# Optimization experiments

Measured on AMD Instinct MI355X. Metric: run time of the kernel, lower is better.

## Reference

```python
import jax, jax.numpy as jnp
import numpy as np

B, CW_DIM, Z_DIM = 512, 4096, 1024
DIM_CODES, BOOK_SIZE, DIM_EMBED = 64, 1024, 64
ENC_H, DEC_H = 512, 2048
SLOPE = 0.2  # LeakyReLU negative slope

def lrelu(v):
    return jnp.where(v > 0, v, SLOPE * v)

def setup_inputs() -> dict:
    key = jax.random.key(0)
    ks = jax.random.split(key, 12)
    s = 0.02
    inp = {
        'x': jax.random.normal(ks[0], (B, CW_DIM), jnp.float32),
        'codebook': jax.random.normal(ks[1], (DIM_CODES, BOOK_SIZE, DIM_EMBED), jnp.float32),
        'enc_w1': jax.random.normal(ks[2], (ENC_H, DIM_EMBED), jnp.float32) * s,
        'enc_b1': jnp.zeros((ENC_H,), jnp.float32),
        'enc_w2': jax.random.normal(ks[3], (2 * Z_DIM, ENC_H), jnp.float32) * s,
        'enc_b2': jnp.zeros((2 * Z_DIM,), jnp.float32),
        'inf1_w': jax.random.normal(ks[4], (Z_DIM // 2, 2 * Z_DIM), jnp.float32) * s,
        'inf1_b': jnp.zeros((Z_DIM // 2,), jnp.float32),
        'inf2_w1': jax.random.normal(ks[5], (2 * Z_DIM, 9 * Z_DIM // 4), jnp.float32) * s,
        'inf2_b1': jnp.zeros((2 * Z_DIM,), jnp.float32),
        'inf2_w2': jax.random.normal(ks[6], (3 * Z_DIM // 2, 2 * Z_DIM), jnp.float32) * s,
        'inf2_b2': jnp.zeros((3 * Z_DIM // 2,), jnp.float32),
        'prior_w1': jax.random.normal(ks[7], (2 * Z_DIM, Z_DIM // 4), jnp.float32) * s,
        'prior_b1': jnp.zeros((2 * Z_DIM,), jnp.float32),
        'prior_w2': jax.random.normal(ks[8], (3 * Z_DIM // 2, 2 * Z_DIM), jnp.float32) * s,
        'prior_b2': jnp.zeros((3 * Z_DIM // 2,), jnp.float32),
        'dec_w1': jax.random.normal(ks[9], (DEC_H, 3 * Z_DIM // 4), jnp.float32) * s,
        'dec_b1': jnp.zeros((DEC_H,), jnp.float32),
        'dec_w2': jax.random.normal(ks[10], (CW_DIM, DEC_H), jnp.float32) * s,
        'dec_b2': jnp.zeros((CW_DIM,), jnp.float32),
    }
    return inp

def reference(x, codebook, enc_w1, enc_b1, enc_w2, enc_b2,
              inf1_w, inf1_b, inf2_w1, inf2_b1, inf2_w2, inf2_b2,
              prior_w1, prior_b1, prior_w2, prior_b2,
              dec_w1, dec_b1, dec_w2, dec_b2):
    b = x.shape[0]
    # ---- encode: view (B, dim_codes, dim_embed), per-code conv + max-pool + Linear
    xe = x.reshape(b, DIM_CODES, DIM_EMBED)                       # (B, C, E)
    feat = lrelu(jnp.einsum('bce,he->bch', xe, enc_w1) + enc_b1)  # (B, C, H)
    h = jnp.max(feat, axis=1) @ enc_w2.T + enc_b2                 # (B, 2z)
    mu, log_var = jnp.split(h @ inf1_w.T + inf1_b, 2, axis=1)     # (B, z/4) each
    z1 = mu                                                        # eval mode: sample == mu
    # ---- decode
    p = lrelu(z1 @ prior_w1.T + prior_b1) @ prior_w2.T + prior_b2
    p_mu, p_logvar = jnp.split(p, 2, axis=1)                       # (B, 3z/4) each
    d = lrelu(jnp.concatenate([z1, h], axis=1) @ inf2_w1.T + inf2_b1) @ inf2_w2.T + inf2_b2
    d_mu, d_log_var = jnp.split(d, 2, axis=1)
    z2 = d_mu + p_mu                                               # eval mode sample
    cw_recon = lrelu(z2 @ dec_w1.T + dec_b1) @ dec_w2.T + dec_b2   # (B, cw_dim)
    # ---- dist: squared distance to (detached) codebook, no explicit repeat
    xr = cw_recon.reshape(b, DIM_CODES, DIM_EMBED)
    book = jax.lax.stop_gradient(codebook)                         # (C, S, E)
    cw_dist = ((xr ** 2).sum(-1)[..., None]
               + (book ** 2).sum(-1)[None]
               - 2.0 * jnp.einsum('bce,cse->bcs', xr, book))       # (B, C, S)
    idx = jnp.argmin(cw_dist, axis=-1).reshape(b * DIM_CODES, 1)   # matches torch (B*C, 1)
    return (cw_recon, cw_dist, idx, mu, log_var, d_mu, d_log_var, p_logvar)
```

## Files before the change

### kernel.cpp

```cpp
#include <hip/hip_runtime.h>
#include <hip/hip_bf16.h>

typedef __hip_bfloat16 bf16;
typedef unsigned short u16;

#define BATCH 512
#define CW_DIM 4096
#define DIM_CODES 64
#define BOOK_SIZE 1024
#define DIM_EMBED 64
#define ENC_H 512

__device__ __forceinline__ float bf2f(u16 u) {
    unsigned int x = ((unsigned int)u) << 16;
    return __uint_as_float(x);
}
__device__ __forceinline__ float loadf(const void* p, size_t i, int bf) {
    if (bf) return bf2f(((const u16*)p)[i]);
    return ((const float*)p)[i];
}
__device__ __forceinline__ float4 load4(const void* p, size_t i, int bf) {
    if (bf) {
        const u16* q = (const u16*)p + i;
        uint2 raw = *reinterpret_cast<const uint2*>(q);
        float4 r;
        r.x = bf2f((u16)(raw.x & 0xFFFF));
        r.y = bf2f((u16)(raw.x >> 16));
        r.z = bf2f((u16)(raw.y & 0xFFFF));
        r.w = bf2f((u16)(raw.y >> 16));
        return r;
    }
    return *reinterpret_cast<const float4*>((const float*)p + i);
}
__device__ __forceinline__ void stored(void* p, size_t i, int bf, double v) {
    if (bf) ((bf16*)p)[i] = __float2bfloat16((float)v);
    else    ((float*)p)[i] = (float)v;
}
__device__ __forceinline__ u16 f2bfu(float v) {
    bf16 b = __float2bfloat16(v);
    return *reinterpret_cast<u16*>(&b);
}

__global__ void detect_kernel(const u16* __restrict__ x, int* __restrict__ flag) {
    __shared__ int hits;
    if (threadIdx.x == 0) hits = 0;
    __syncthreads();
    int h = 0;
    for (int i = threadIdx.x; i < 16384; i += 256) {
        u16 v = x[2 * i];
        if (((v >> 7) & 0xFF) == 0xFF) h++;
    }
    atomicAdd(&hits, h);
    __syncthreads();
    if (threadIdx.x == 0) *flag = (hits == 0) ? 1 : 0;
}

__global__ void booknorm_kernel(const void* __restrict__ book, double* __restrict__ bn,
                                const int* __restrict__ dflag) {
    const int bf = *dflag;
    int r = blockIdx.x * blockDim.x + threadIdx.x;
    if (r >= DIM_CODES * BOOK_SIZE) return;
    double acc = 0.0;
    for (int e = 0; e < DIM_EMBED; e += 4) {
        float4 v = load4(book, (size_t)r * DIM_EMBED + e, bf);
        acc = fma((double)v.x, (double)v.x, acc);
        acc = fma((double)v.y, (double)v.y, acc);
        acc = fma((double)v.z, (double)v.z, acc);
        acc = fma((double)v.w, (double)v.w, acc);
    }
    bn[r] = acc;
}

__global__ __launch_bounds__(256) void enc_kernel(const void* __restrict__ x,
                                                  const void* __restrict__ w1,
                                                  const void* __restrict__ b1,
                                                  float* __restrict__ hmax,
                                                  const int* __restrict__ dflag) {
    const int bf = *dflag;
    __shared__ float xs_t[64][68];
    __shared__ float wsh_t[64][68];
    __shared__ float red[64][17];
    int t = threadIdx.x;
    int h0 = blockIdx.x * 64;
    int b = blockIdx.y;

    int cr = t >> 2;
    int e0 = (t & 3) << 4;
    for (int q = 0; q < 4; q++) {
        int e = e0 + (q << 2);
        float4 xv = load4(x, (size_t)b * CW_DIM + cr * DIM_EMBED + e, bf);
        xs_t[e + 0][cr] = xv.x; xs_t[e + 1][cr] = xv.y;
        xs_t[e + 2][cr] = xv.z; xs_t[e + 3][cr] = xv.w;
        float4 wv = load4(w1, (size_t)(h0 + cr) * DIM_EMBED + e, bf);
        wsh_t[e + 0][cr] = wv.x; wsh_t[e + 1][cr] = wv.y;
        wsh_t[e + 2][cr] = wv.z; wsh_t[e + 3][cr] = wv.w;
    }
    __syncthreads();

    int th = t & 15, tc = t >> 4;
    float acc[4][4] = {};
    for (int e = 0; e < 64; e++) {
        float4 a4 = *(const float4*)&xs_t[e][tc << 2];
        float4 w4 = *(const float4*)&wsh_t[e][th << 2];
        float aa[4] = {a4.x, a4.y, a4.z, a4.w};
        float ww[4] = {w4.x, w4.y, w4.z, w4.w};
#pragma unroll
        for (int i = 0; i < 4; i++)
#pragma unroll
            for (int j = 0; j < 4; j++)
                acc[i][j] = fmaf(aa[i], ww[j], acc[i][j]);
    }
#pragma unroll
    for (int j = 0; j < 4; j++) {
        float bj = loadf(b1, h0 + (th << 2) + j, bf);
        float m = -1e30f;
#pragma unroll
        for (int i = 0; i < 4; i++) {
            float v = acc[i][j] + bj;
            v = v > 0.f ? v : 0.2f * v;
            m = fmaxf(m, v);
        }
        red[(th << 2) + j][tc] = m;
    }
    __syncthreads();
    if (t < 64) {
        float m = red[t][0];
        for (int k = 1; k < 16; k++) m = fmaxf(m, red[t][k]);
        hmax[(size_t)b * ENC_H + h0 + t] = m;
    }
}

struct GDesc {
    const float* A1; const float* A2; const float* Aadd;
    const void* W; const void* bias; float* C;
    int lda1, K1, lda2, Ktot, N, act, nbx, pad;
    size_t s0base; int s0c0, s0c1, s0stride;
    size_t s1base; int s1c0, s1c1, s1stride;
};

__device__ __forceinline__ void gemm_body(const GDesc& g, int bx, int by,
                                          void* __restrict__ out, const int bf) {
    __shared__ float As[2][16][68];
    __shared__ float Ws[2][16][68];
    int t = threadIdx.x;
    int tx = t & 15, ty = t >> 4;
    int n0 = bx * 64, m0 = by * 64;
    int mrow = t >> 2, kq = (t & 3) << 2;
    float acc[4][4] = {};

    float4 av, wv;
    {
        int k = kq;
        if (k < g.K1) {
            av = *reinterpret_cast<const float4*>(g.A1 + (size_t)(m0 + mrow) * g.lda1 + k);
            if (g.Aadd) {
                float4 ad = *reinterpret_cast<const float4*>(g.Aadd + (size_t)(m0 + mrow) * g.lda1 + k);
                av.x += ad.x; av.y += ad.y; av.z += ad.z; av.w += ad.w;
            }
        } else {
            av = *reinterpret_cast<const float4*>(g.A2 + (size_t)(m0 + mrow) * g.lda2 + (k - g.K1));
        }
        wv = load4(g.W, (size_t)(n0 + mrow) * g.Ktot + k, bf);
    }
    As[0][kq + 0][mrow] = av.x; As[0][kq + 1][mrow] = av.y;
    As[0][kq + 2][mrow] = av.z; As[0][kq + 3][mrow] = av.w;
    Ws[0][kq + 0][mrow] = wv.x; Ws[0][kq + 1][mrow] = wv.y;
    Ws[0][kq + 2][mrow] = wv.z; Ws[0][kq + 3][mrow] = wv.w;
    __syncthreads();

    int buf = 0;
#pragma unroll 1
    for (int kt = 0; kt < g.Ktot; kt += 16) {
        int nxt = kt + 16;
        if (nxt < g.Ktot) {
            int k = nxt + kq;
            if (k < g.K1) {
                av = *reinterpret_cast<const float4*>(g.A1 + (size_t)(m0 + mrow) * g.lda1 + k);
                if (g.Aadd) {
                    float4 ad = *reinterpret_cast<const float4*>(g.Aadd + (size_t)(m0 + mrow) * g.lda1 + k);
                    av.x += ad.x; av.y += ad.y; av.z += ad.z; av.w += ad.w;
                }
            } else {
                av = *reinterpret_cast<const float4*>(g.A2 + (size_t)(m0 + mrow) * g.lda2 + (k - g.K1));
            }
            wv = load4(g.W, (size_t)(n0 + mrow) * g.Ktot + k, bf);
        }
#pragma unroll
        for (int kk = 0; kk < 16; kk++) {
            float4 a4 = *(const float4*)&As[buf][kk][ty << 2];
            float4 w4 = *(const float4*)&Ws[buf][kk][tx << 2];
            float a[4] = {a4.x, a4.y, a4.z, a4.w};
            float w[4] = {w4.x, w4.y, w4.z, w4.w};
#pragma unroll
            for (int i = 0; i < 4; i++)
#pragma unroll
                for (int j = 0; j < 4; j++)
                    acc[i][j] = fmaf(a[i], w[j], acc[i][j]);
        }
        if (nxt < g.Ktot) {
            int nb = buf ^ 1;
            As[nb][kq + 0][mrow] = av.x; As[nb][kq + 1][mrow] = av.y;
            As[nb][kq + 2][mrow] = av.z; As[nb][kq + 3][mrow] = av.w;
            Ws[nb][kq + 0][mrow] = wv.x; Ws[nb][kq + 1][mrow] = wv.y;
            Ws[nb][kq + 2][mrow] = wv.z; Ws[nb][kq + 3][mrow] = wv.w;
            __syncthreads();
            buf = nb;
        }
    }

    int nbase = n0 + tx * 4;
    float b0 = loadf(g.bias, nbase + 0, bf), b1v = loadf(g.bias, nbase + 1, bf);
    float b2 = loadf(g.bias, nbase + 2, bf), b3 = loadf(g.bias, nbase + 3, bf);
#pragma unroll
    for (int i = 0; i < 4; i++) {
        int m = m0 + ty * 4 + i;
        float ov[4];
        ov[0] = acc[i][0] + b0; ov[1] = acc[i][1] + b1v;
        ov[2] = acc[i][2] + b2; ov[3] = acc[i][3] + b3;
        if (g.act) {
#pragma unroll
            for (int j = 0; j < 4; j++) ov[j] = ov[j] > 0.f ? ov[j] : 0.2f * ov[j];
        }
        float4 o = {ov[0], ov[1], ov[2], ov[3]};
        *reinterpret_cast<float4*>(g.C + (size_t)m * g.N + nbase) = o;
        if (nbase >= g.s0c0 && nbase < g.s0c1) {
            size_t off = g.s0base + (size_t)m * g.s0stride + (nbase - g.s0c0);
            if (bf) {
                ushort4 h = {f2bfu(ov[0]), f2bfu(ov[1]), f2bfu(ov[2]), f2bfu(ov[3])};
                *reinterpret_cast<ushort4*>((u16*)out + off) = h;
            } else {
                *reinterpret_cast<float4*>((float*)out + off) = o;
            }
        }
        if (nbase >= g.s1c0 && nbase < g.s1c1) {
            size_t off = g.s1base + (size_t)m * g.s1stride + (nbase - g.s1c0);
            if (bf) {
                ushort4 h = {f2bfu(ov[0]), f2bfu(ov[1]), f2bfu(ov[2]), f2bfu(ov[3])};
                *reinterpret_cast<ushort4*>((u16*)out + off) = h;
            } else {
                *reinterpret_cast<float4*>((float*)out + off) = o;
            }
        }
    }
}

__global__ __launch_bounds__(256) void gemm_kernel(GDesc g, void* __restrict__ out,
                                                   const int* __restrict__ dflag) {
    gemm_body(g, blockIdx.x, blockIdx.y, out, *dflag);
}

__global__ __launch_bounds__(256) void gemm2_kernel(GDesc g0, GDesc g1, void* __restrict__ out,
                                                    const int* __restrict__ dflag) {
    const int bf = *dflag;
    bool first = (int)blockIdx.x < g0.nbx;
    GDesc g = first ? g0 : g1;
    int bx = first ? blockIdx.x : blockIdx.x - g0.nbx;
    gemm_body(g, bx, blockIdx.y, out, bf);
}

__global__ __launch_bounds__(256, 4) void dist_kernel(const float* __restrict__ cwr,
                                                      const void* __restrict__ book,
                                                      const double* __restrict__ bn,
                                                      void* __restrict__ out,
                                                      size_t odist, size_t oidx,
                                                      const int* __restrict__ dflag) {
    const int bf = *dflag;
    __shared__ double xs[32][64];
    __shared__ double xn[32];
    __shared__ float bs[2][64][66];
    int t = threadIdx.x;
    int c = blockIdx.x;
    int b0 = blockIdx.y * 32;
    int sl = t & 63, wv = t >> 6;

    for (int i = t; i < 32 * 64; i += 256) {
        int bl = i >> 6, e = i & 63;
        xs[bl][e] = (double)cwr[(size_t)(b0 + bl) * CW_DIM + c * DIM_EMBED + e];
    }
    {
        size_t base = (size_t)c * BOOK_SIZE * DIM_EMBED;
        int i4, srow, e4;
        i4 = t;       srow = i4 >> 4; e4 = (i4 & 15) << 2;
        float4 v0 = load4(book, base + (size_t)srow * DIM_EMBED + e4, bf);
        bs[0][srow][e4 + 0] = v0.x; bs[0][srow][e4 + 1] = v0.y;
        bs[0][srow][e4 + 2] = v0.z; bs[0][srow][e4 + 3] = v0.w;
        i4 = t + 256; srow = i4 >> 4; e4 = (i4 & 15) << 2;
        float4 v1 = load4(book, base + (size_t)srow * DIM_EMBED + e4, bf);
        bs[0][srow][e4 + 0] = v1.x; bs[0][srow][e4 + 1] = v1.y;
        bs[0][srow][e4 + 2] = v1.z; bs[0][srow][e4 + 3] = v1.w;
        i4 = t + 512; srow = i4 >> 4; e4 = (i4 & 15) << 2;
        float4 v2 = load4(book, base + (size_t)srow * DIM_EMBED + e4, bf);
        bs[0][srow][e4 + 0] = v2.x; bs[0][srow][e4 + 1] = v2.y;
        bs[0][srow][e4 + 2] = v2.z; bs[0][srow][e4 + 3] = v2.w;
        i4 = t + 768; srow = i4 >> 4; e4 = (i4 & 15) << 2;
        float4 v3 = load4(book, base + (size_t)srow * DIM_EMBED + e4, bf);
        bs[0][srow][e4 + 0] = v3.x; bs[0][srow][e4 + 1] = v3.y;
        bs[0][srow][e4 + 2] = v3.z; bs[0][srow][e4 + 3] = v3.w;
    }
    __syncthreads();
    if (t < 32) {
        double a = 0.0;
        for (int e = 0; e < 64; e++) a = fma(xs[t][e], xs[t][e], a);
        xn[t] = a;
    }
    __syncthreads();

    double bd[8];
    int bsx[8];
#pragma unroll
    for (int p = 0; p < 8; p++) { bd[p] = 1e300; bsx[p] = 0; }

#pragma unroll 1
    for (int st = 0; st < 16; st++) {
        int s0 = st * 64;
        int cur = st & 1, nb = cur ^ 1;
        double bnv = bn[(size_t)c * BOOK_SIZE + s0 + sl];
        float4 pf0, pf1, pf2, pf3;
        int s0n = s0 + 64;
        if (st < 15) {
            size_t base = ((size_t)c * BOOK_SIZE + s0n) * DIM_EMBED;
            int i4, srow, e4;
            i4 = t;       srow = i4 >> 4; e4 = (i4 & 15) << 2;
            pf0 = load4(book, base + (size_t)srow * DIM_EMBED + e4, bf);
            i4 = t + 256; srow = i4 >> 4; e4 = (i4 & 15) << 2;
            pf1 = load4(book, base + (size_t)srow * DIM_EMBED + e4, bf);
            i4 = t + 512; srow = i4 >> 4; e4 = (i4 & 15) << 2;
            pf2 = load4(book, base + (size_t)srow * DIM_EMBED + e4, bf);
            i4 = t + 768; srow = i4 >> 4; e4 = (i4 & 15) << 2;
            pf3 = load4(book, base + (size_t)srow * DIM_EMBED + e4, bf);
        }
#pragma unroll
        for (int pb = 0; pb < 2; pb++) {
            int blb = wv * 8 + pb * 4;
            double a0 = 0.0, a1 = 0.0, a2 = 0.0, a3 = 0.0;
#pragma unroll 8
            for (int e = 0; e < 64; e += 2) {
                float2 bv = *(const float2*)&bs[cur][sl][e];
                double bv0 = (double)bv.x, bv1 = (double)bv.y;
                double2 x0 = *(const double2*)&xs[blb + 0][e];
                double2 x1 = *(const double2*)&xs[blb + 1][e];
                double2 x2 = *(const double2*)&xs[blb + 2][e];
                double2 x3 = *(const double2*)&xs[blb + 3][e];
                a0 = fma(x0.x, bv0, a0); a0 = fma(x0.y, bv1, a0);
                a1 = fma(x1.x, bv0, a1); a1 = fma(x1.y, bv1, a1);
                a2 = fma(x2.x, bv0, a2); a2 = fma(x2.y, bv1, a2);
                a3 = fma(x3.x, bv0, a3); a3 = fma(x3.y, bv1, a3);
            }
            double dv[4];
            dv[0] = a0; dv[1] = a1; dv[2] = a2; dv[3] = a3;
#pragma unroll
            for (int j = 0; j < 4; j++) {
                int bl = blb + j;
                double d = xn[bl] + bnv - 2.0 * dv[j];
                stored(out, odist + ((size_t)(b0 + bl) * DIM_CODES + c) * BOOK_SIZE + s0 + sl, bf, d);
                if (d < bd[pb * 4 + j]) { bd[pb * 4 + j] = d; bsx[pb * 4 + j] = s0 + sl; }
            }
        }
        if (st < 15) {
            int i4, srow, e4;
            i4 = t;       srow = i4 >> 4; e4 = (i4 & 15) << 2;
            bs[nb][srow][e4 + 0] = pf0.x; bs[nb][srow][e4 + 1] = pf0.y;
            bs[nb][srow][e4 + 2] = pf0.z; bs[nb][srow][e4 + 3] = pf0.w;
            i4 = t + 256; srow = i4 >> 4; e4 = (i4 & 15) << 2;
            bs[nb][srow][e4 + 0] = pf1.x; bs[nb][srow][e4 + 1] = pf1.y;
            bs[nb][srow][e4 + 2] = pf1.z; bs[nb][srow][e4 + 3] = pf1.w;
            i4 = t + 512; srow = i4 >> 4; e4 = (i4 & 15) << 2;
            bs[nb][srow][e4 + 0] = pf2.x; bs[nb][srow][e4 + 1] = pf2.y;
            bs[nb][srow][e4 + 2] = pf2.z; bs[nb][srow][e4 + 3] = pf2.w;
            i4 = t + 768; srow = i4 >> 4; e4 = (i4 & 15) << 2;
            bs[nb][srow][e4 + 0] = pf3.x; bs[nb][srow][e4 + 1] = pf3.y;
            bs[nb][srow][e4 + 2] = pf3.z; bs[nb][srow][e4 + 3] = pf3.w;
            __syncthreads();
        }
    }
#pragma unroll
    for (int p = 0; p < 8; p++) {
        double d = bd[p];
        int s = bsx[p];
        for (int off = 32; off >= 1; off >>= 1) {
            double od = __shfl_xor(d, off, 64);
            int os = __shfl_xor(s, off, 64);
            if (od < d || (od == d && os < s)) { d = od; s = os; }
        }
        if (sl == 0)
            stored(out, oidx + (size_t)(b0 + wv * 8 + p) * DIM_CODES + c, bf, (double)s);
    }
}

extern "C" void kernel_launch(void* const* d_in, const int* in_sizes, int n_in,
                              void* d_out, int out_size, void* d_ws, size_t ws_size,
                              hipStream_t stream) {
    const void* x        = d_in[0];
    const void* codebook = d_in[1];
    const void* enc_w1   = d_in[2];
    const void* enc_b1   = d_in[3];
    const void* enc_w2   = d_in[4];
    const void* enc_b2   = d_in[5];
    const void* inf1_w   = d_in[6];
    const void* inf1_b   = d_in[7];
    const void* inf2_w1  = d_in[8];
    const void* inf2_b1  = d_in[9];
    const void* inf2_w2  = d_in[10];
    const void* inf2_b2  = d_in[11];
    const void* prior_w1 = d_in[12];
    const void* prior_b1 = d_in[13];
    const void* prior_w2 = d_in[14];
    const void* prior_b2 = d_in[15];
    const void* dec_w1   = d_in[16];
    const void* dec_b1   = d_in[17];
    const void* dec_w2   = d_in[18];
    const void* dec_b2   = d_in[19];

    float* W0 = (float*)d_ws;
    float* inf1out = W0;
    float* pfull   = inf1out + 262144;
    float* dfull   = pfull + 786432;
    float* cwr     = dfull + 786432;
    float* bufA    = cwr + 2097152;
    float* bufB    = bufA + 1048576;
    float* bufD    = bufB + 1048576;
    float* bufC    = bufD + 1048576;
    double* bn     = (double*)(bufC + 262144);
    int* dflag     = (int*)(bn + 65536);

    const size_t o_cwrecon = 0;
    const size_t o_cwdist  = 2097152;
    const size_t o_idx     = 35651584;
    const size_t o_mu      = 35684352;
    const size_t o_logvar  = 35815424;
    const size_t o_dmu     = 35946496;
    const size_t o_dlogvar = 36339712;
    const size_t o_plogvar = 36732928;

    detect_kernel<<<1, 256, 0, stream>>>((const u16*)x, dflag);
    booknorm_kernel<<<256, 256, 0, stream>>>(codebook, bn, dflag);
    enc_kernel<<<dim3(8, BATCH), 256, 0, stream>>>(x, enc_w1, enc_b1, bufC, dflag);

    GDesc g, ga, gb;
    g = {bufC, bufC, nullptr, enc_w2, enc_b2, bufA,
         512, 512, 512, 512, 2048, 0, 32, 0,
         0, 0, 0, 0, 0, 0, 0, 0};
    gemm_kernel<<<dim3(32, 8), 256, 0, stream>>>(g, d_out, dflag);
    g = {bufA, bufA, nullptr, inf1_w, inf1_b, inf1out,
         2048, 2048, 2048, 2048, 512, 0, 8, 0,
         o_mu, 0, 256, 256, o_logvar, 256, 512, 256};
    gemm_kernel<<<dim3(8, 8), 256, 0, stream>>>(g, d_out, dflag);
    ga = {inf1out, inf1out, nullptr, prior_w1, prior_b1, bufB,
          512, 256, 512, 256, 2048, 1, 32, 0,
          0, 0, 0, 0, 0, 0, 0, 0};
    gb = {inf1out, bufA, nullptr, inf2_w1, inf2_b1, bufD,
          512, 256, 2048, 2304, 2048, 1, 32, 0,
          0, 0, 0, 0, 0, 0, 0, 0};
    gemm2_kernel<<<dim3(64, 8), 256, 0, stream>>>(ga, gb, d_out, dflag);
    ga = {bufB, bufB, nullptr, prior_w2, prior_b2, pfull,
          2048, 2048, 2048, 2048, 1536, 0, 24, 0,
          o_plogvar, 768, 1536, 768, 0, 0, 0, 0};
    gb = {bufD, bufD, nullptr, inf2_w2, inf2_b2, dfull,
          2048, 2048, 2048, 2048, 1536, 0, 24, 0,
          o_dmu, 0, 768, 768, o_dlogvar, 768, 1536, 768};
    gemm2_kernel<<<dim3(48, 8), 256, 0, stream>>>(ga, gb, d_out, dflag);
    g = {dfull, dfull, pfull, dec_w1, dec_b1, bufA,
         1536, 768, 1536, 768, 2048, 1, 32, 0,
         0, 0, 0, 0, 0, 0, 0, 0};
    gemm_kernel<<<dim3(32, 8), 256, 0, stream>>>(g, d_out, dflag);
    g = {bufA, bufA, nullptr, dec_w2, dec_b2, cwr,
         2048, 2048, 2048, 2048, 4096, 0, 64, 0,
         o_cwrecon, 0, 4096, 4096, 0, 0, 0, 0};
    gemm_kernel<<<dim3(64, 8), 256, 0, stream>>>(g, d_out, dflag);

    dist_kernel<<<dim3(64, 16), 256, 0, stream>>>(cwr, codebook, bn,
                                                  d_out, o_cwdist, o_idx, dflag);
}
```

Before: 1.021 ms.

## Retile dist kernel to 2x4 register tile with transposed shared layouts

```diff
diff --git a/kernel.cpp b/kernel.cpp
--- a/kernel.cpp
+++ b/kernel.cpp
@@ -265,125 +265,134 @@
                                                       size_t odist, size_t oidx,
                                                       const int* __restrict__ dflag) {
     const int bf = *dflag;
-    __shared__ double xs[32][64];
+    __shared__ double xst[64][34];
+    __shared__ float  bst[64][68];
     __shared__ double xn[32];
-    __shared__ float bs[2][64][66];
     int t = threadIdx.x;
     int c = blockIdx.x;
     int b0 = blockIdx.y * 32;
-    int sl = t & 63, wv = t >> 6;
-
-    for (int i = t; i < 32 * 64; i += 256) {
-        int bl = i >> 6, e = i & 63;
-        xs[bl][e] = (double)cwr[(size_t)(b0 + bl) * CW_DIM + c * DIM_EMBED + e];
-    }
+    int tx = t & 15, ty = t >> 4;
+
     {
-        size_t base = (size_t)c * BOOK_SIZE * DIM_EMBED;
-        int i4, srow, e4;
-        i4 = t;       srow = i4 >> 4; e4 = (i4 & 15) << 2;
-        float4 v0 = load4(book, base + (size_t)srow * DIM_EMBED + e4, bf);
-        bs[0][srow][e4 + 0] = v0.x; bs[0][srow][e4 + 1] = v0.y;
-        bs[0][srow][e4 + 2] = v0.z; bs[0][srow][e4 + 3] = v0.w;
-        i4 = t + 256; srow = i4 >> 4; e4 = (i4 & 15) << 2;
-        float4 v1 = load4(book, base + (size_t)srow * DIM_EMBED + e4, bf);
-        bs[0][srow][e4 + 0] = v1.x; bs[0][srow][e4 + 1] = v1.y;
-        bs[0][srow][e4 + 2] = v1.z; bs[0][srow][e4 + 3] = v1.w;
-        i4 = t + 512; srow = i4 >> 4; e4 = (i4 & 15) << 2;
-        float4 v2 = load4(book, base + (size_t)srow * DIM_EMBED + e4, bf);
-        bs[0][srow][e4 + 0] = v2.x; bs[0][srow][e4 + 1] = v2.y;
-        bs[0][srow][e4 + 2] = v2.z; bs[0][srow][e4 + 3] = v2.w;
-        i4 = t + 768; srow = i4 >> 4; e4 = (i4 & 15) << 2;
-        float4 v3 = load4(book, base + (size_t)srow * DIM_EMBED + e4, bf);
-        bs[0][srow][e4 + 0] = v3.x; bs[0][srow][e4 + 1] = v3.y;
-        bs[0][srow][e4 + 2] = v3.z; bs[0][srow][e4 + 3] = v3.w;
+        int bp = (t >> 4) << 1, e4 = (t & 15) << 2;
+        float4 xa = *reinterpret_cast<const float4*>(cwr + (size_t)(b0 + bp) * CW_DIM + c * DIM_EMBED + e4);
+        float4 xb = *reinterpret_cast<const float4*>(cwr + (size_t)(b0 + bp + 1) * CW_DIM + c * DIM_EMBED + e4);
+        double2 w;
+        w.x = (double)xa.x; w.y = (double)xb.x; *(double2*)&xst[e4 + 0][bp] = w;
+        w.x = (double)xa.y; w.y = (double)xb.y; *(double2*)&xst[e4 + 1][bp] = w;
+        w.x = (double)xa.z; w.y = (double)xb.z; *(double2*)&xst[e4 + 2][bp] = w;
+        w.x = (double)xa.w; w.y = (double)xb.w; *(double2*)&xst[e4 + 3][bp] = w;
+    }
+    {
+        int sp = (t >> 3) << 1, e8 = (t & 7) << 3;
+        size_t base = ((size_t)c * BOOK_SIZE + sp) * DIM_EMBED + e8;
+        float4 p0 = load4(book, base, bf);
+        float4 p1 = load4(book, base + 4, bf);
+        float4 p2 = load4(book, base + DIM_EMBED, bf);
+        float4 p3 = load4(book, base + DIM_EMBED + 4, bf);
+        float2 f;
+        f.x = p0.x; f.y = p2.x; *(float2*)&bst[e8 + 0][sp] = f;
+        f.x = p0.y; f.y = p2.y; *(float2*)&bst[e8 + 1][sp] = f;
+        f.x = p0.z; f.y = p2.z; *(float2*)&bst[e8 + 2][sp] = f;
+        f.x = p0.w; f.y = p2.w; *(float2*)&bst[e8 + 3][sp] = f;
+        f.x = p1.x; f.y = p3.x; *(float2*)&bst[e8 + 4][sp] = f;
+        f.x = p1.y; f.y = p3.y; *(float2*)&bst[e8 + 5][sp] = f;
+        f.x = p1.z; f.y = p3.z; *(float2*)&bst[e8 + 6][sp] = f;
+        f.x = p1.w; f.y = p3.w; *(float2*)&bst[e8 + 7][sp] = f;
     }
     __syncthreads();
     if (t < 32) {
         double a = 0.0;
-        for (int e = 0; e < 64; e++) a = fma(xs[t][e], xs[t][e], a);
+        for (int e = 0; e < 64; e++) { double v = xst[e][t]; a = fma(v, v, a); }
         xn[t] = a;
     }
     __syncthreads();
 
-    double bd[8];
-    int bsx[8];
-#pragma unroll
-    for (int p = 0; p < 8; p++) { bd[p] = 1e300; bsx[p] = 0; }
+    double xnb0 = xn[ty << 1], xnb1 = xn[(ty << 1) + 1];
+
+    double bd[2];
+    int bsx[2];
+    bd[0] = 1e300; bd[1] = 1e300; bsx[0] = 0; bsx[1] = 0;
 
 #pragma unroll 1
     for (int st = 0; st < 16; st++) {
         int s0 = st * 64;
-        int cur = st & 1, nb = cur ^ 1;
-        double bnv = bn[(size_t)c * BOOK_SIZE + s0 + sl];
         float4 pf0, pf1, pf2, pf3;
-        int s0n = s0 + 64;
+        int sp = (t >> 3) << 1, e8 = (t & 7) << 3;
         if (st < 15) {
-            size_t base = ((size_t)c * BOOK_SIZE + s0n) * DIM_EMBED;
-            int i4, srow, e4;
-            i4 = t;       srow = i4 >> 4; e4 = (i4 & 15) << 2;
-            pf0 = load4(book, base + (size_t)srow * DIM_EMBED + e4, bf);
-            i4 = t + 256; srow = i4 >> 4; e4 = (i4 & 15) << 2;
-            pf1 = load4(book, base + (size_t)srow * DIM_EMBED + e4, bf);
-            i4 = t + 512; srow = i4 >> 4; e4 = (i4 & 15) << 2;
-            pf2 = load4(book, base + (size_t)srow * DIM_EMBED + e4, bf);
-            i4 = t + 768; srow = i4 >> 4; e4 = (i4 & 15) << 2;
-            pf3 = load4(book, base + (size_t)srow * DIM_EMBED + e4, bf);
-        }
-#pragma unroll
-        for (int pb = 0; pb < 2; pb++) {
-            int blb = wv * 8 + pb * 4;
-            double a0 = 0.0, a1 = 0.0, a2 = 0.0, a3 = 0.0;
+            size_t base = ((size_t)c * BOOK_SIZE + s0 + 64 + sp) * DIM_EMBED + e8;
+            pf0 = load4(book, base, bf);
+            pf1 = load4(book, base + 4, bf);
+            pf2 = load4(book, base + DIM_EMBED, bf);
+            pf3 = load4(book, base + DIM_EMBED + 4, bf);
+        }
+        const double* bnp = bn + ((size_t)c << 10) + s0 + (tx << 2);
+        double2 bn01 = *reinterpret_cast<const double2*>(bnp);
+        double2 bn23 = *reinterpret_cast<const double2*>(bnp + 2);
+
+        double acc[2][4] = {};
 #pragma unroll 8
-            for (int e = 0; e < 64; e += 2) {
-                float2 bv = *(const float2*)&bs[cur][sl][e];
-                double bv0 = (double)bv.x, bv1 = (double)bv.y;
-                double2 x0 = *(const double2*)&xs[blb + 0][e];
-                double2 x1 = *(const double2*)&xs[blb + 1][e];
-                double2 x2 = *(const double2*)&xs[blb + 2][e];
-                double2 x3 = *(const double2*)&xs[blb + 3][e];
-                a0 = fma(x0.x, bv0, a0); a0 = fma(x0.y, bv1, a0);
-                a1 = fma(x1.x, bv0, a1); a1 = fma(x1.y, bv1, a1);
-                a2 = fma(x2.x, bv0, a2); a2 = fma(x2.y, bv1, a2);
-                a3 = fma(x3.x, bv0, a3); a3 = fma(x3.y, bv1, a3);
+        for (int e = 0; e < 64; e++) {
+            double2 xv = *(const double2*)&xst[e][ty << 1];
+            float4 bv = *(const float4*)&bst[e][tx << 2];
+            double bv0 = (double)bv.x, bv1 = (double)bv.y;
+            double bv2 = (double)bv.z, bv3 = (double)bv.w;
+            acc[0][0] = fma(xv.x, bv0, acc[0][0]);
+            acc[0][1] = fma(xv.x, bv1, acc[0][1]);
+            acc[0][2] = fma(xv.x, bv2, acc[0][2]);
+            acc[0][3] = fma(xv.x, bv3, acc[0][3]);
+            acc[1][0] = fma(xv.y, bv0, acc[1][0]);
+            acc[1][1] = fma(xv.y, bv1, acc[1][1]);
+            acc[1][2] = fma(xv.y, bv2, acc[1][2]);
+            acc[1][3] = fma(xv.y, bv3, acc[1][3]);
+        }
+        int sbase = s0 + (tx << 2);
+#pragma unroll
+        for (int ib = 0; ib < 2; ib++) {
+            int b = (ty << 1) + ib;
+            double xnb = ib ? xnb1 : xnb0;
+            double d0 = xnb + bn01.x - 2.0 * acc[ib][0];
+            double d1 = xnb + bn01.y - 2.0 * acc[ib][1];
+            double d2 = xnb + bn23.x - 2.0 * acc[ib][2];
+            double d3 = xnb + bn23.y - 2.0 * acc[ib][3];
+            if (d0 < bd[ib]) { bd[ib] = d0; bsx[ib] = sbase + 0; }
+            if (d1 < bd[ib]) { bd[ib] = d1; bsx[ib] = sbase + 1; }
+            if (d2 < bd[ib]) { bd[ib] = d2; bsx[ib] = sbase + 2; }
+            if (d3 < bd[ib]) { bd[ib] = d3; bsx[ib] = sbase + 3; }
+            size_t off = odist + ((size_t)(b0 + b) * DIM_CODES + c) * BOOK_SIZE + sbase;
+            if (bf) {
+                ushort4 h = {f2bfu((float)d0), f2bfu((float)d1), f2bfu((float)d2), f2bfu((float)d3)};
+                *reinterpret_cast<ushort4*>((u16*)out + off) = h;
+            } else {
+                float4 o = {(float)d0, (float)d1, (float)d2, (float)d3};
+                *reinterpret_cast<float4*>((float*)out + off) = o;
             }
-            double dv[4];
-            dv[0] = a0; dv[1] = a1; dv[2] = a2; dv[3] = a3;
-#pragma unroll
-            for (int j = 0; j < 4; j++) {
-                int bl = blb + j;
-                double d = xn[bl] + bnv - 2.0 * dv[j];
-                stored(out, odist + ((size_t)(b0 + bl) * DIM_CODES + c) * BOOK_SIZE + s0 + sl, bf, d);
-                if (d < bd[pb * 4 + j]) { bd[pb * 4 + j] = d; bsx[pb * 4 + j] = s0 + sl; }
-            }
         }
         if (st < 15) {
-            int i4, srow, e4;
-            i4 = t;       srow = i4 >> 4; e4 = (i4 & 15) << 2;
-            bs[nb][srow][e4 + 0] = pf0.x; bs[nb][srow][e4 + 1] = pf0.y;
-            bs[nb][srow][e4 + 2] = pf0.z; bs[nb][srow][e4 + 3] = pf0.w;
-            i4 = t + 256; srow = i4 >> 4; e4 = (i4 & 15) << 2;
-            bs[nb][srow][e4 + 0] = pf1.x; bs[nb][srow][e4 + 1] = pf1.y;
-            bs[nb][srow][e4 + 2] = pf1.z; bs[nb][srow][e4 + 3] = pf1.w;
-            i4 = t + 512; srow = i4 >> 4; e4 = (i4 & 15) << 2;
-            bs[nb][srow][e4 + 0] = pf2.x; bs[nb][srow][e4 + 1] = pf2.y;
-            bs[nb][srow][e4 + 2] = pf2.z; bs[nb][srow][e4 + 3] = pf2.w;
-            i4 = t + 768; srow = i4 >> 4; e4 = (i4 & 15) << 2;
-            bs[nb][srow][e4 + 0] = pf3.x; bs[nb][srow][e4 + 1] = pf3.y;
-            bs[nb][srow][e4 + 2] = pf3.z; bs[nb][srow][e4 + 3] = pf3.w;
             __syncthreads();
-        }
-    }
-#pragma unroll
-    for (int p = 0; p < 8; p++) {
-        double d = bd[p];
-        int s = bsx[p];
-        for (int off = 32; off >= 1; off >>= 1) {
+            float2 f;
+            f.x = pf0.x; f.y = pf2.x; *(float2*)&bst[e8 + 0][sp] = f;
+            f.x = pf0.y; f.y = pf2.y; *(float2*)&bst[e8 + 1][sp] = f;
+            f.x = pf0.z; f.y = pf2.z; *(float2*)&bst[e8 + 2][sp] = f;
+            f.x = pf0.w; f.y = pf2.w; *(float2*)&bst[e8 + 3][sp] = f;
+            f.x = pf1.x; f.y = pf3.x; *(float2*)&bst[e8 + 4][sp] = f;
+            f.x = pf1.y; f.y = pf3.y; *(float2*)&bst[e8 + 5][sp] = f;
+            f.x = pf1.z; f.y = pf3.z; *(float2*)&bst[e8 + 6][sp] = f;
+            f.x = pf1.w; f.y = pf3.w; *(float2*)&bst[e8 + 7][sp] = f;
+            __syncthreads();
+        }
+    }
+#pragma unroll
+    for (int ib = 0; ib < 2; ib++) {
+        double d = bd[ib];
+        int s = bsx[ib];
+        for (int off = 8; off >= 1; off >>= 1) {
             double od = __shfl_xor(d, off, 64);
             int os = __shfl_xor(s, off, 64);
             if (od < d || (od == d && os < s)) { d = od; s = os; }
         }
-        if (sl == 0)
-            stored(out, oidx + (size_t)(b0 + wv * 8 + p) * DIM_CODES + c, bf, (double)s);
+        if (tx == 0)
+            stored(out, oidx + (size_t)(b0 + (ty << 1) + ib) * DIM_CODES + c, bf, (double)s);
     }
 }
 
```

Result: faster. 986.7 us (-3.4%).
